# Optimization experiments

Measured on AMD Instinct MI355X. Metric: run time of the kernel, lower is better.

Reference implementation:

```python
import jax, jax.numpy as jnp
import numpy as np

INPUT_SIZE = 2048
HIDDEN_SIZE = 4096
OUTPUT_SIZE = 2048
T = 2048


def setup_inputs() -> dict:
    key = jax.random.key(0)
    kx, k1, k2, k3 = jax.random.split(key, 4)
    x = jax.random.normal(kx, (T, INPUT_SIZE), dtype=jnp.float32)
    # Xavier-style init matching the torch module
    sx = np.sqrt(2.0 / (INPUT_SIZE + HIDDEN_SIZE)).astype(np.float32)
    sh = np.sqrt(2.0 / (HIDDEN_SIZE + OUTPUT_SIZE)).astype(np.float32)
    Wx = jax.random.normal(k1, (HIDDEN_SIZE, INPUT_SIZE), dtype=jnp.float32) * sx
    Wh = jax.random.normal(k2, (HIDDEN_SIZE, OUTPUT_SIZE), dtype=jnp.float32) * sh
    Wy = jax.random.normal(k3, (OUTPUT_SIZE, HIDDEN_SIZE), dtype=jnp.float32) * sh
    bh = jnp.zeros((HIDDEN_SIZE,), dtype=jnp.float32)
    by = jnp.zeros((OUTPUT_SIZE,), dtype=jnp.float32)
    return {"x": x, "Wx": Wx, "Wh": Wh, "Wy": Wy, "bh": bh, "by": by}


def reference(x, Wx, Wh, Wy, bh, by):
    # Jordan RNN: h_t = tanh(Wx@x_t + Wh@y_{t-1} + bh); y_t = Wy@h_t + by
    def step(y_prev, x_t):
        h = jnp.tanh(Wx @ x_t + Wh @ y_prev + bh)
        y = Wy @ h + by
        return y, y

    y0 = jnp.zeros((OUTPUT_SIZE,), dtype=x.dtype)
    _, ys = jax.lax.scan(step, y0, x)  # ys: [T, output_size]
    return ys.reshape(-1)
```

## Files before the change

kernel.cpp:

```cpp
#include <hip/hip_runtime.h>


#define T_STEPS 2048
#define HID 4096
#define NIN 2048
#define NOUT 2048
#define SENT 0x7F807F80u

typedef unsigned short u16;
typedef unsigned int u32;
typedef __attribute__((ext_vector_type(8))) short bf16x8;
typedef __attribute__((ext_vector_type(4))) float f32x4;

__device__ __forceinline__ u16 f2b(float f) {
  u32 u = __float_as_uint(f);
  u32 r = (u + 0x7fffu + ((u >> 16) & 1u)) >> 16;
  return (u16)r;
}
__device__ __forceinline__ float b2f(u16 h) { return __uint_as_float(((u32)h) << 16); }

__global__ void conv_kernel(const float* __restrict__ in, u16* __restrict__ out, int n4) {
  int stride = gridDim.x * blockDim.x;
  for (int i = blockIdx.x * blockDim.x + threadIdx.x; i < n4; i += stride) {
    float4 v = *reinterpret_cast<const float4*>(in + (size_t)i * 4);
    uint2 p;
    p.x = (u32)f2b(v.x) | ((u32)f2b(v.y) << 16);
    p.y = (u32)f2b(v.z) | ((u32)f2b(v.w) << 16);
    *reinterpret_cast<uint2*>(out + (size_t)i * 4) = p;
  }
}

__global__ void fill_kernel(u32* __restrict__ p, u32 val, int n16) {
  int stride = gridDim.x * blockDim.x;
  uint4 v = {val, val, val, val};
  for (int i = blockIdx.x * blockDim.x + threadIdx.x; i < n16; i += stride)
    reinterpret_cast<uint4*>(p)[i] = v;
}

__global__ void transpose_conv(const float* __restrict__ in, u16* __restrict__ out, int R, int C) {
  __shared__ float tile[32][33];
  int bx = blockIdx.x * 32;
  int by = blockIdx.y * 32;
  int tx = threadIdx.x & 31, ty = threadIdx.x >> 5;
#pragma unroll
  for (int k = 0; k < 32; k += 8)
    tile[ty + k][tx] = in[(size_t)(by + ty + k) * C + bx + tx];
  __syncthreads();
#pragma unroll
  for (int k = 0; k < 32; k += 8)
    out[(size_t)(bx + ty + k) * R + by + tx] = f2b(tile[tx][ty + k]);
}

__global__ void cvec_kernel(const float* __restrict__ Wh, const float* __restrict__ by,
                            float* __restrict__ c) {
  int k = blockIdx.x, l = threadIdx.x;
  float s = 0.f;
  for (int i = l; i < NOUT; i += 64) s += Wh[(size_t)k * NOUT + i] * by[i];
#pragma unroll
  for (int m = 32; m; m >>= 1) s += __shfl_xor(s, m, 64);
  if (l == 0) c[k] = s;
}

__global__ __launch_bounds__(256) void gemm_bt(
    const u16* __restrict__ A, const u16* __restrict__ Bt,
    int M, int N, int K,
    float* __restrict__ Cf, u16* __restrict__ Cb,
    const float* __restrict__ bias) {
  __shared__ __align__(16) u16 As[64][40];
  __shared__ __align__(16) u16 Bs[64][40];
  const int tid = threadIdx.x;
  const int wave = tid >> 6;
  const int lane = tid & 63;
  const int m0 = blockIdx.y * 64;
  const int n0 = blockIdx.x * 64;
  const int lr = tid >> 2;
  const int lc = (tid & 3) << 3;
  const int frow = lane & 15;
  const int koff = (lane >> 4) << 3;

  f32x4 acc0 = {0.f, 0.f, 0.f, 0.f};
  f32x4 acc1 = acc0, acc2 = acc0, acc3 = acc0;

  const u16* pA = A + (size_t)(m0 + lr) * K + lc;
  const u16* pB = Bt + (size_t)(n0 + lr) * K + lc;

  for (int k0 = 0; k0 < K; k0 += 32) {
    uint4 va = *reinterpret_cast<const uint4*>(pA + k0);
    uint4 vb = *reinterpret_cast<const uint4*>(pB + k0);
    *reinterpret_cast<uint4*>(&As[lr][lc]) = va;
    *reinterpret_cast<uint4*>(&Bs[lr][lc]) = vb;
    __syncthreads();
    bf16x8 af = *reinterpret_cast<const bf16x8*>(&As[(wave << 4) + frow][koff]);
    bf16x8 b0 = *reinterpret_cast<const bf16x8*>(&Bs[frow][koff]);
    bf16x8 b1 = *reinterpret_cast<const bf16x8*>(&Bs[16 + frow][koff]);
    bf16x8 b2 = *reinterpret_cast<const bf16x8*>(&Bs[32 + frow][koff]);
    bf16x8 b3 = *reinterpret_cast<const bf16x8*>(&Bs[48 + frow][koff]);
    acc0 = __builtin_amdgcn_mfma_f32_16x16x32_bf16(af, b0, acc0, 0, 0, 0);
    acc1 = __builtin_amdgcn_mfma_f32_16x16x32_bf16(af, b1, acc1, 0, 0, 0);
    acc2 = __builtin_amdgcn_mfma_f32_16x16x32_bf16(af, b2, acc2, 0, 0, 0);
    acc3 = __builtin_amdgcn_mfma_f32_16x16x32_bf16(af, b3, acc3, 0, 0, 0);
    __syncthreads();
  }

  const int crow = m0 + (wave << 4) + ((lane >> 4) << 2);
  const int ccol = n0 + (lane & 15);
  float bv0 = bias ? bias[ccol] : 0.f;
  float bv1 = bias ? bias[ccol + 16] : 0.f;
  float bv2 = bias ? bias[ccol + 32] : 0.f;
  float bv3 = bias ? bias[ccol + 48] : 0.f;
  if (Cf) {
#pragma unroll
    for (int r = 0; r < 4; ++r) {
      size_t base = (size_t)(crow + r) * N + ccol;
      Cf[base] = acc0[r] + bv0;
      Cf[base + 16] = acc1[r] + bv1;
      Cf[base + 32] = acc2[r] + bv2;
      Cf[base + 48] = acc3[r] + bv3;
    }
  } else {
#pragma unroll
    for (int r = 0; r < 4; ++r) {
      size_t base = (size_t)(crow + r) * N + ccol;
      Cb[base] = f2b(acc0[r] + bv0);
      Cb[base + 16] = f2b(acc1[r] + bv1);
      Cb[base + 32] = f2b(acc2[r] + bv2);
      Cb[base + 48] = f2b(acc3[r] + bv3);
    }
  }
}

__global__ __launch_bounds__(512, 2) void seq_kernel(
    const u16* __restrict__ Wm, const u16* __restrict__ Zb,
    const float* __restrict__ cvec, u16* __restrict__ H, int T) {
  const int tid = threadIdx.x;
  const int b = blockIdx.x;
  const int r0 = b * 16;

  float w[16][8];
  {
    const u16* wp = Wm + (size_t)r0 * HID + tid * 8;
#pragma unroll
    for (int r = 0; r < 16; ++r) {
      uint4 q = *reinterpret_cast<const uint4*>(wp + (size_t)r * HID);
      w[r][0] = __uint_as_float(q.x << 16);
      w[r][1] = __uint_as_float(q.x & 0xffff0000u);
      w[r][2] = __uint_as_float(q.y << 16);
      w[r][3] = __uint_as_float(q.y & 0xffff0000u);
      w[r][4] = __uint_as_float(q.z << 16);
      w[r][5] = __uint_as_float(q.z & 0xffff0000u);
      w[r][6] = __uint_as_float(q.w << 16);
      w[r][7] = __uint_as_float(q.w & 0xffff0000u);
    }
  }
  const int rgrp = tid >> 5;
  const int ilane = tid & 31;
  const int wv = tid >> 6;
  const int lane = tid & 63;
  const float c_r = cvec[r0 + rgrp];

  __shared__ float red[512][17];

  const u32* Hu = reinterpret_cast<const u32*>(H);
  u32* Hw = reinterpret_cast<u32*>(H);

  for (int t = 1; t <= T; ++t) {
    float zv = 0.f;
    if (ilane == 0) zv = b2f(Zb[(size_t)(t - 1) * HID + r0 + rgrp]);

    float acc[16];
#pragma unroll
    for (int r = 0; r < 16; ++r) acc[r] = 0.f;

    if (t >= 2) {
      const u32* hrow = Hu + (size_t)(t - 2) * (HID / 2) + tid * 4;
      u32 q0, q1, q2, q3;
      for (;;) {
        q0 = __hip_atomic_load(hrow + 0, __ATOMIC_RELAXED, __HIP_MEMORY_SCOPE_AGENT);
        q1 = __hip_atomic_load(hrow + 1, __ATOMIC_RELAXED, __HIP_MEMORY_SCOPE_AGENT);
        q2 = __hip_atomic_load(hrow + 2, __ATOMIC_RELAXED, __HIP_MEMORY_SCOPE_AGENT);
        q3 = __hip_atomic_load(hrow + 3, __ATOMIC_RELAXED, __HIP_MEMORY_SCOPE_AGENT);
        if (q0 != SENT && q1 != SENT && q2 != SENT && q3 != SENT) break;
      }
      float h[8];
      h[0] = __uint_as_float(q0 << 16); h[1] = __uint_as_float(q0 & 0xffff0000u);
      h[2] = __uint_as_float(q1 << 16); h[3] = __uint_as_float(q1 & 0xffff0000u);
      h[4] = __uint_as_float(q2 << 16); h[5] = __uint_as_float(q2 & 0xffff0000u);
      h[6] = __uint_as_float(q3 << 16); h[7] = __uint_as_float(q3 & 0xffff0000u);
#pragma unroll
      for (int c = 0; c < 8; ++c) {
#pragma unroll
        for (int r = 0; r < 16; ++r) acc[r] = fmaf(w[r][c], h[c], acc[r]);
      }
    }

#pragma unroll
    for (int r = 0; r < 16; ++r) red[tid][r] = acc[r];
    __syncthreads();

    float s = 0.f;
#pragma unroll
    for (int p = 0; p < 16; ++p) s += red[ilane + 32 * p][rgrp];
    s += __shfl_xor(s, 16, 64);
    s += __shfl_xor(s, 8, 64);
    s += __shfl_xor(s, 4, 64);
    s += __shfl_xor(s, 2, 64);
    s += __shfl_xor(s, 1, 64);

    float pre = zv + s + ((t >= 2) ? c_r : 0.f);
    float ax = fabsf(pre);
    float e = __expf(2.f * ax);
    float th = 1.f - 2.f / (e + 1.f);
    float hv = (pre < 0.f) ? -th : th;
    float hv2 = __shfl_xor(hv, 32, 64);

    if (lane == 0) {
      u32 pk = (u32)f2b(hv) | ((u32)f2b(hv2) << 16);
      __hip_atomic_store(Hw + (size_t)(t - 1) * (HID / 2) + (r0 >> 1) + wv, pk,
                         __ATOMIC_RELAXED, __HIP_MEMORY_SCOPE_AGENT);
    }
    __syncthreads();
  }
}

extern "C" void kernel_launch(void* const* d_in, const int* in_sizes, int n_in,
                              void* d_out, int out_size, void* d_ws, size_t ws_size,
                              hipStream_t stream) {
  (void)in_sizes; (void)n_in; (void)out_size; (void)ws_size;
  const float* x  = (const float*)d_in[0];
  const float* Wx = (const float*)d_in[1];
  const float* Wh = (const float*)d_in[2];
  const float* Wy = (const float*)d_in[3];
  const float* bh = (const float*)d_in[4];
  const float* by = (const float*)d_in[5];
  float* out = (float*)d_out;

  char* ws = (char*)d_ws;
  const size_t MB = 1ull << 20;
  u16* Whb  = (u16*)(ws + 0 * MB);
  u16* WyTb = (u16*)(ws + 16 * MB);
  u16* Wyb  = (u16*)(ws + 32 * MB);
  u16* Zb   = (u16*)(ws + 48 * MB);
  u16* Hb   = (u16*)(ws + 64 * MB);
  u16* xb   = (u16*)(ws + 80 * MB);
  u16* Wxb  = (u16*)(ws + 88 * MB);
  u16* Wmb  = (u16*)(ws + 80 * MB);
  float* cv = (float*)(ws + 112 * MB);

  conv_kernel<<<1024, 256, 0, stream>>>(x, xb, (T_STEPS * NIN) / 4);
  conv_kernel<<<1024, 256, 0, stream>>>(Wx, Wxb, (HID * NIN) / 4);
  conv_kernel<<<1024, 256, 0, stream>>>(Wh, Whb, (HID * NOUT) / 4);
  conv_kernel<<<1024, 256, 0, stream>>>(Wy, Wyb, (NOUT * HID) / 4);
  transpose_conv<<<dim3(HID / 32, NOUT / 32), 256, 0, stream>>>(Wy, WyTb, NOUT, HID);
  cvec_kernel<<<HID, 64, 0, stream>>>(Wh, by, cv);
  fill_kernel<<<1024, 256, 0, stream>>>((u32*)Hb, SENT, (T_STEPS * HID) / 8);

  gemm_bt<<<dim3(HID / 64, T_STEPS / 64), 256, 0, stream>>>(
      xb, Wxb, T_STEPS, HID, NIN, nullptr, Zb, bh);
  gemm_bt<<<dim3(HID / 64, HID / 64), 256, 0, stream>>>(
      Whb, WyTb, HID, HID, NOUT, nullptr, Wmb, nullptr);

  int T = T_STEPS;
  void* args[] = {(void*)&Wmb, (void*)&Zb, (void*)&cv, (void*)&Hb, (void*)&T};
  hipLaunchCooperativeKernel((const void*)seq_kernel, dim3(256), dim3(512), args, 0, stream);

  gemm_bt<<<dim3(NOUT / 64, T_STEPS / 64), 256, 0, stream>>>(
      Hb, Wyb, T_STEPS, NOUT, HID, out, nullptr, by);
}
```

Baseline: 4.583 ms.

## Restructure recurrent kernel to per-wave rows with LDS flag sync and dot2

Each wavefront now owns two output rows and keeps its packed bf16 weights in registers, using v_dot2_f32_bf16 instead of unpacking to fp32 FMAs. The previous hidden vector is loaded cooperatively into a double-buffered LDS array. Waves coordinate through workgroup-scope flags instead of __syncthreads, and each row's sum is reduced with wave shuffles rather than a shared-memory reduction. This cuts register pressure, LDS traffic and barrier cost on the serial critical path. It relies on inline asm and custom spin-wait ordering, which adds correctness risk.

```diff
diff --git a/kernel.cpp b/kernel.cpp
--- a/kernel.cpp
+++ b/kernel.cpp
@@ -11,6 +11,9 @@
 typedef unsigned int u32;
 typedef __attribute__((ext_vector_type(8))) short bf16x8;
 typedef __attribute__((ext_vector_type(4))) float f32x4;
+
+#define DOT2(acc, w_, h_) \
+  asm("v_dot2_f32_bf16 %0, %1, %2, %0" : "+v"(acc) : "v"(w_), "v"(h_))
 
 __device__ __forceinline__ u16 f2b(float f) {
   u32 u = __float_as_uint(f);
@@ -133,92 +136,110 @@
     const u16* __restrict__ Wm, const u16* __restrict__ Zb,
     const float* __restrict__ cvec, u16* __restrict__ H, int T) {
   const int tid = threadIdx.x;
+  const int lane = tid & 63;
+  const int wv = tid >> 6;
   const int b = blockIdx.x;
-  const int r0 = b * 16;
-
-  float w[16][8];
+  const int r0 = b * 16 + wv * 2;
+
+  uint4 wp0[8], wp1[8];
   {
-    const u16* wp = Wm + (size_t)r0 * HID + tid * 8;
-#pragma unroll
-    for (int r = 0; r < 16; ++r) {
-      uint4 q = *reinterpret_cast<const uint4*>(wp + (size_t)r * HID);
-      w[r][0] = __uint_as_float(q.x << 16);
-      w[r][1] = __uint_as_float(q.x & 0xffff0000u);
-      w[r][2] = __uint_as_float(q.y << 16);
-      w[r][3] = __uint_as_float(q.y & 0xffff0000u);
-      w[r][4] = __uint_as_float(q.z << 16);
-      w[r][5] = __uint_as_float(q.z & 0xffff0000u);
-      w[r][6] = __uint_as_float(q.w << 16);
-      w[r][7] = __uint_as_float(q.w & 0xffff0000u);
-    }
-  }
-  const int rgrp = tid >> 5;
-  const int ilane = tid & 31;
-  const int wv = tid >> 6;
-  const int lane = tid & 63;
-  const float c_r = cvec[r0 + rgrp];
-
-  __shared__ float red[512][17];
+    const u16* wr = Wm + (size_t)r0 * HID + (lane << 3);
+#pragma unroll
+    for (int c = 0; c < 8; ++c) {
+      wp0[c] = *reinterpret_cast<const uint4*>(wr + (c << 9));
+      wp1[c] = *reinterpret_cast<const uint4*>(wr + HID + (c << 9));
+    }
+  }
+  const float c0 = cvec[r0];
+  const float c1 = cvec[r0 + 1];
+
+  __shared__ __align__(16) u32 hbuf[2][HID / 2];
+  __shared__ u32 flags[2][8];
+  if (tid < 16) reinterpret_cast<u32*>(flags)[tid] = 0;
+  __syncthreads();
 
   const u32* Hu = reinterpret_cast<const u32*>(H);
   u32* Hw = reinterpret_cast<u32*>(H);
-
-  for (int t = 1; t <= T; ++t) {
-    float zv = 0.f;
-    if (ilane == 0) zv = b2f(Zb[(size_t)(t - 1) * HID + r0 + rgrp]);
-
-    float acc[16];
-#pragma unroll
-    for (int r = 0; r < 16; ++r) acc[r] = 0.f;
-
-    if (t >= 2) {
-      const u32* hrow = Hu + (size_t)(t - 2) * (HID / 2) + tid * 4;
-      u32 q0, q1, q2, q3;
-      for (;;) {
-        q0 = __hip_atomic_load(hrow + 0, __ATOMIC_RELAXED, __HIP_MEMORY_SCOPE_AGENT);
-        q1 = __hip_atomic_load(hrow + 1, __ATOMIC_RELAXED, __HIP_MEMORY_SCOPE_AGENT);
-        q2 = __hip_atomic_load(hrow + 2, __ATOMIC_RELAXED, __HIP_MEMORY_SCOPE_AGENT);
-        q3 = __hip_atomic_load(hrow + 3, __ATOMIC_RELAXED, __HIP_MEMORY_SCOPE_AGENT);
-        if (q0 != SENT && q1 != SENT && q2 != SENT && q3 != SENT) break;
-      }
-      float h[8];
-      h[0] = __uint_as_float(q0 << 16); h[1] = __uint_as_float(q0 & 0xffff0000u);
-      h[2] = __uint_as_float(q1 << 16); h[3] = __uint_as_float(q1 & 0xffff0000u);
-      h[4] = __uint_as_float(q2 << 16); h[5] = __uint_as_float(q2 & 0xffff0000u);
-      h[6] = __uint_as_float(q3 << 16); h[7] = __uint_as_float(q3 & 0xffff0000u);
-#pragma unroll
-      for (int c = 0; c < 8; ++c) {
-#pragma unroll
-        for (int r = 0; r < 16; ++r) acc[r] = fmaf(w[r][c], h[c], acc[r]);
-      }
-    }
-
-#pragma unroll
-    for (int r = 0; r < 16; ++r) red[tid][r] = acc[r];
-    __syncthreads();
-
-    float s = 0.f;
-#pragma unroll
-    for (int p = 0; p < 16; ++p) s += red[ilane + 32 * p][rgrp];
-    s += __shfl_xor(s, 16, 64);
-    s += __shfl_xor(s, 8, 64);
-    s += __shfl_xor(s, 4, 64);
-    s += __shfl_xor(s, 2, 64);
-    s += __shfl_xor(s, 1, 64);
-
-    float pre = zv + s + ((t >= 2) ? c_r : 0.f);
+  const u32* Zu = reinterpret_cast<const u32*>(Zb);
+  const int slot = (b << 3) + wv;
+
+  {
+    u32 zq = Zu[slot];
+    float pre0 = __uint_as_float(zq << 16);
+    float pre1 = __uint_as_float(zq & 0xffff0000u);
+    float pre = (lane & 1) ? pre1 : pre0;
     float ax = fabsf(pre);
     float e = __expf(2.f * ax);
     float th = 1.f - 2.f / (e + 1.f);
-    float hv = (pre < 0.f) ? -th : th;
-    float hv2 = __shfl_xor(hv, 32, 64);
-
+    th = (pre < 0.f) ? -th : th;
+    float tho = __shfl_xor(th, 1, 64);
     if (lane == 0) {
-      u32 pk = (u32)f2b(hv) | ((u32)f2b(hv2) << 16);
-      __hip_atomic_store(Hw + (size_t)(t - 1) * (HID / 2) + (r0 >> 1) + wv, pk,
+      u32 pk = (u32)f2b(th) | ((u32)f2b(tho) << 16);
+      __hip_atomic_store(Hw + slot, pk, __ATOMIC_RELAXED, __HIP_MEMORY_SCOPE_AGENT);
+    }
+  }
+
+  for (int t = 2; t <= T; ++t) {
+    const int p = (t - 1) & 1;
+    u32 zq = Zu[(size_t)(t - 1) * (HID / 2) + slot];
+
+    const u32* hsrc = Hu + (size_t)(t - 2) * (HID / 2) + (wv << 8) + (lane << 2);
+    u32 q0, q1, q2, q3;
+    for (;;) {
+      q0 = __hip_atomic_load(hsrc + 0, __ATOMIC_RELAXED, __HIP_MEMORY_SCOPE_AGENT);
+      q1 = __hip_atomic_load(hsrc + 1, __ATOMIC_RELAXED, __HIP_MEMORY_SCOPE_AGENT);
+      q2 = __hip_atomic_load(hsrc + 2, __ATOMIC_RELAXED, __HIP_MEMORY_SCOPE_AGENT);
+      q3 = __hip_atomic_load(hsrc + 3, __ATOMIC_RELAXED, __HIP_MEMORY_SCOPE_AGENT);
+      if (q0 != SENT && q1 != SENT && q2 != SENT && q3 != SENT) break;
+    }
+
+    {
+      uint4 st = {q0, q1, q2, q3};
+      *reinterpret_cast<uint4*>(&hbuf[p][(wv << 8) + (lane << 2)]) = st;
+      if (lane == 0)
+        __hip_atomic_store(&flags[p][wv], (u32)t, __ATOMIC_RELEASE,
+                           __HIP_MEMORY_SCOPE_WORKGROUP);
+    }
+
+    for (;;) {
+      bool ok = true;
+#pragma unroll
+      for (int r = 0; r < 8; ++r)
+        ok &= (__hip_atomic_load(&flags[p][r], __ATOMIC_RELAXED,
+                                 __HIP_MEMORY_SCOPE_WORKGROUP) >= (u32)t);
+      if (ok) break;
+    }
+    __builtin_amdgcn_fence(__ATOMIC_ACQUIRE, "workgroup");
+
+    float a0 = 0.f, a1 = 0.f;
+#pragma unroll
+    for (int c = 0; c < 8; ++c) {
+      uint4 hq = *reinterpret_cast<const uint4*>(&hbuf[p][(c << 8) + (lane << 2)]);
+      DOT2(a0, wp0[c].x, hq.x); DOT2(a0, wp0[c].y, hq.y);
+      DOT2(a0, wp0[c].z, hq.z); DOT2(a0, wp0[c].w, hq.w);
+      DOT2(a1, wp1[c].x, hq.x); DOT2(a1, wp1[c].y, hq.y);
+      DOT2(a1, wp1[c].z, hq.z); DOT2(a1, wp1[c].w, hq.w);
+    }
+
+#pragma unroll
+    for (int m = 32; m; m >>= 1) {
+      a0 += __shfl_xor(a0, m, 64);
+      a1 += __shfl_xor(a1, m, 64);
+    }
+
+    float pre0 = a0 + __uint_as_float(zq << 16) + c0;
+    float pre1 = a1 + __uint_as_float(zq & 0xffff0000u) + c1;
+    float pre = (lane & 1) ? pre1 : pre0;
+    float ax = fabsf(pre);
+    float e = __expf(2.f * ax);
+    float th = 1.f - 2.f / (e + 1.f);
+    th = (pre < 0.f) ? -th : th;
+    float tho = __shfl_xor(th, 1, 64);
+    if (lane == 0) {
+      u32 pk = (u32)f2b(th) | ((u32)f2b(tho) << 16);
+      __hip_atomic_store(Hw + (size_t)(t - 1) * (HID / 2) + slot, pk,
                          __ATOMIC_RELAXED, __HIP_MEMORY_SCOPE_AGENT);
     }
-    __syncthreads();
   }
 }
 
```

Measured after the change: 13.44 ms. 193% more time.
